# Optimization experiments

Hardware: AMD Instinct MI355X
Metric: run time of the kernel (lower is better)

The kernel has to match this reference:

```python
import jax, jax.numpy as jnp
import numpy as np

DIM = 256
HEADS = 8
W0, W1 = 8, 8
N = W0 * W1
SCALE = (DIM // HEADS) ** (-0.5)


def _rel_pos_index(w0, w1):
    ch = np.arange(w0)
    cw = np.arange(w1)
    coords = np.stack(np.meshgrid(ch, cw, indexing='ij')).reshape(2, -1)  # (2, N)
    rel = coords[:, :, None] - coords[:, None, :]                          # (2, N, N)
    rel = rel.transpose(1, 2, 0).copy()                                    # (N, N, 2)
    rel[:, :, 0] += w0 - 1
    rel[:, :, 1] += w1 - 1
    rel[:, :, 0] *= 2 * w1 - 1
    return rel.sum(-1)                                                     # (N, N)

REL_IDX = jnp.asarray(_rel_pos_index(W0, W1))


def setup_inputs() -> dict:
    key = jax.random.key(0)
    ks = jax.random.split(key, 9)
    B, C, H, W = 8, DIM, 128, 128
    s = DIM ** -0.5
    return {
        'x': jax.random.normal(ks[0], (B, C, H, W), jnp.float32),
        'embedding': jax.random.normal(ks[1], (1, N, DIM), jnp.float32),
        'rpb_table': jax.random.normal(ks[2], ((2 * W0 - 1) * (2 * W1 - 1), HEADS), jnp.float32),
        'q_w': jax.random.normal(ks[3], (DIM, DIM), jnp.float32) * s,
        'q_b': jnp.zeros((DIM,), jnp.float32),
        'kv_w': jax.random.normal(ks[4], (2 * DIM, DIM), jnp.float32) * s,
        'kv_b': jnp.zeros((2 * DIM,), jnp.float32),
        'proj_w': jax.random.normal(ks[5], (DIM, DIM), jnp.float32) * s,
        'proj_b': jnp.zeros((DIM,), jnp.float32),
    }


def reference(x, embedding, rpb_table, q_w, q_b, kv_w, kv_b, proj_w, proj_b):
    B, C, H, W = x.shape
    # window_partition (faithful to the original, incl. its discarded-permute view):
    # torch views the contiguous (B,C,H,W) buffer as (B, H//w0, w0, W//w1, w1, C)
    win = x.reshape(B, H // W0, W0, W // W1, W1, C)
    win = win.transpose(0, 1, 3, 2, 4, 5).reshape(-1, N, C)  # (Bw, N, C)
    Bw = win.shape[0]
    hd = C // HEADS

    q = jnp.einsum('bnc,dc->bnd', jnp.broadcast_to(embedding, (Bw, N, C)), q_w) + q_b
    q = q.reshape(Bw, N, HEADS, hd).transpose(0, 2, 1, 3)      # (Bw, h, N, hd)
    kv = jnp.einsum('bnc,dc->bnd', win, kv_w) + kv_b           # (Bw, N, 2C)
    kv = kv.reshape(Bw, N, 2, HEADS, hd).transpose(2, 0, 3, 1, 4)
    k, v = kv[0], kv[1]                                         # (Bw, h, N, hd)

    bias = rpb_table[REL_IDX.reshape(-1)].reshape(N, N, HEADS).transpose(2, 0, 1)  # (h, N, N)

    attn = jnp.einsum('bhnd,bhmd->bhnm', q * SCALE, k) + bias[None]
    attn = jax.nn.softmax(attn, axis=-1)
    out = jnp.einsum('bhnm,bhmd->bhnd', attn, v)
    out = out.transpose(0, 2, 1, 3).reshape(Bw, N, C)
    out = jnp.einsum('bnc,dc->bnd', out, proj_w) + proj_b
    return out
```

## Files before the change

### kernel.cpp

```cpp
#include <hip/hip_runtime.h>

typedef short bf16x8 __attribute__((ext_vector_type(8)));
typedef float f32x4 __attribute__((ext_vector_type(4)));
typedef float f32x16 __attribute__((ext_vector_type(16)));
typedef unsigned u32;
typedef unsigned short u16;
typedef unsigned u32x4v __attribute__((ext_vector_type(4)));
typedef unsigned u32x2v __attribute__((ext_vector_type(2)));

union UV { u32x4v u; bf16x8 v; };

__device__ __forceinline__ u16 f2bf(float f){
  u32 u = __float_as_uint(f);
  u += 0x7FFFu + ((u>>16)&1u);
  return (u16)(u>>16);
}
__device__ __forceinline__ u32 pack2(float lo, float hi){
  u32 r;
  asm("v_cvt_pk_bf16_f32 %0, %1, %2" : "=v"(r) : "v"(lo), "v"(hi));
  return r;
}

#define LOG2E 1.4426950408889634f

__global__ void k_prep(const float* __restrict__ emb, const float* __restrict__ q_w,
                       const float* __restrict__ q_b, u16* __restrict__ q_s,
                       const float* __restrict__ rpb, float* __restrict__ bias,
                       const float* __restrict__ kv_w, const float* __restrict__ proj_w,
                       u32* __restrict__ kvb, u32* __restrict__ pjb){
  const int blk = blockIdx.x, tid = threadIdx.x;
  if(blk < 64){
    const int n = blk, d = tid;
    const float4* er = (const float4*)(emb + n*256);
    const float4* wr = (const float4*)(q_w + d*256);
    float acc = 0.f;
    for(int c=0;c<64;++c){
      float4 e = er[c], w = wr[c];
      acc += e.x*w.x + e.y*w.y + e.z*w.z + e.w*w.w;
    }
    acc += q_b[d];
    q_s[n*256 + d] = f2bf(acc * (0.17677669529663687f * LOG2E));
  } else if(blk < 192){
    const int o = (blk-64)*256 + tid;
    const int h = o>>12, n = (o>>6)&63, m = o&63;
    const int idx = ((n>>3)-(m>>3)+7)*15 + ((n&7)-(m&7)+7);
    bias[o] = rpb[idx*8 + h] * LOG2E;
  } else {
    const int i = (blk-192)*256 + tid;
    if(i < 65536) kvb[i] = pack2(kv_w[2*i], kv_w[2*i+1]);
    else { int j = i - 65536; pjb[j] = pack2(proj_w[2*j], proj_w[2*j+1]); }
  }
}

__global__ __launch_bounds__(512,4) void k_fused(const float* __restrict__ x, const u16* __restrict__ kvw,
                                                 const float* __restrict__ kv_b, const u16* __restrict__ q_s,
                                                 const float* __restrict__ bias, const u16* __restrict__ pjw,
                                                 const float* __restrict__ proj_b, float* __restrict__ out){
  __shared__ char smem[65536];
  char* RA = smem;
  char* RB = smem + 32768;

  const int bw = blockIdx.x;
  const int b = bw>>8, h1 = (bw>>4)&15, w1 = bw&15;
  const int base = b*4194304 + h1*262144 + w1*2048;
  const int tid = threadIdx.x;
  const int w = tid>>6, l = tid&63, g = l>>4, li = l&15;
  const int l31 = l&31, hi = l>>5;

  const u16* wbase = kvw + (w*64 + li)*256 + g*8;
  bf16x8 bcur[4];
  #pragma unroll
  for(int ct=0;ct<4;++ct) bcur[ct] = *(const bf16x8*)(wbase + ct*4096);

  #pragma unroll
  for(int i=0;i<4;++i){
    int p = i*512 + tid;
    int n = p>>5;
    int c4 = (2*p)&63;
    const f32x4* gp = (const f32x4*)(x + base + (n>>3)*32768 + (n&7)*256 + c4*4);
    f32x4 lo = __builtin_nontemporal_load(gp);
    f32x4 hh = __builtin_nontemporal_load(gp+1);
    u32x4v d = { pack2(lo[0],lo[1]), pack2(lo[2],lo[3]), pack2(hh[0],hh[1]), pack2(hh[2],hh[3]) };
    *(u32x4v*)(RA + ((p*16) ^ ((n&7)<<4))) = d;
  }
  __syncthreads();

  f32x4 acc[4][4];
  #pragma unroll
  for(int ct=0;ct<4;++ct){
    float bv = kv_b[w*64 + ct*16 + li];
    #pragma unroll
    for(int rt=0;rt<4;++rt) acc[rt][ct] = (f32x4){bv,bv,bv,bv};
  }
  {
    __builtin_amdgcn_s_setprio(1);
    #pragma unroll
    for(int ks=0;ks<8;++ks){
      bf16x8 a[4];
      #pragma unroll
      for(int rt=0;rt<4;++rt){
        int n = rt*16 + li;
        a[rt] = *(const bf16x8*)(RA + ((n*512 + ks*64 + g*16) ^ ((n&7)<<4)));
      }
      #pragma unroll
      for(int ct=0;ct<4;++ct){
        #pragma unroll
        for(int rt=0;rt<4;++rt)
          acc[rt][ct] = __builtin_amdgcn_mfma_f32_16x16x32_bf16(a[rt], bcur[ct], acc[rt][ct], 0,0,0);
        if(ks<7) bcur[ct] = *(const bf16x8*)(wbase + ct*4096 + (ks+1)*32);
      }
    }
    __builtin_amdgcn_s_setprio(0);
  }
  __syncthreads();

  const int h = w;
  bf16x8 qf[2][2];
  #pragma unroll
  for(int nt=0;nt<2;++nt)
    #pragma unroll
    for(int ks=0;ks<2;++ks)
      qf[nt][ks] = *(const bf16x8*)(q_s + (nt*32 + l31)*256 + h*32 + ks*16 + hi*8);

  const int oddl = li & 1;
  if(w < 4){
    #pragma unroll
    for(int ct=0;ct<4;++ct){
      int colp = w*64 + ct*16 + (li & ~1);
      #pragma unroll
      for(int rt=0;rt<4;++rt){
        float v0=acc[rt][ct][0], v1=acc[rt][ct][1], v2=acc[rt][ct][2], v3=acc[rt][ct][3];
        float o0=__shfl_xor(v0,1), o1=__shfl_xor(v1,1), o2=__shfl_xor(v2,1), o3=__shfl_xor(v3,1);
        u32 d0 = oddl ? pack2(o2,v2) : pack2(v0,o0);
        u32 d1 = oddl ? pack2(o3,v3) : pack2(v1,o1);
        int row0 = rt*16 + 4*g + (oddl ? 2 : 0);
        *(u32*)(RA + ((row0*512     + colp*2) ^ ((row0&7)<<4)))     = d0;
        *(u32*)(RA + (((row0+1)*512 + colp*2) ^ (((row0+1)&7)<<4))) = d1;
      }
    }
  } else {
    #pragma unroll
    for(int ct=0;ct<4;++ct){
      int c2 = (w-4)*64 + ct*16 + li;
      int hv = c2>>5, e = c2&31;
      #pragma unroll
      for(int rt=0;rt<4;++rt){
        u32x2v d;
        d[0] = pack2(acc[rt][ct][0], acc[rt][ct][1]);
        d[1] = pack2(acc[rt][ct][2], acc[rt][ct][3]);
        int m0 = rt*16 + 4*g;
        *(u32x2v*)(RB + (((hv*32 + e)*128 + m0*2) ^ ((e&7)<<4))) = d;
      }
    }
  }
  __syncthreads();

  bf16x8 kf[2][2];
  #pragma unroll
  for(int mt=0;mt<2;++mt)
    #pragma unroll
    for(int ks=0;ks<2;++ks){
      int row = mt*32 + l31;
      kf[mt][ks] = *(const bf16x8*)(RA + ((row*512 + (h*32 + ks*16 + hi*8)*2) ^ ((row&7)<<4)));
    }

  f32x16 S[2][2];
  #pragma unroll
  for(int mt=0;mt<2;++mt)
    #pragma unroll
    for(int nt=0;nt<2;++nt){
      int n = nt*32 + l31;
      const float* bp = bias + h*4096 + n*64 + mt*32 + 4*hi;
      #pragma unroll
      for(int q=0;q<4;++q){
        float4 bv = *(const float4*)(bp + q*8);
        S[mt][nt][4*q+0] = bv.x; S[mt][nt][4*q+1] = bv.y;
        S[mt][nt][4*q+2] = bv.z; S[mt][nt][4*q+3] = bv.w;
      }
    }
  __builtin_amdgcn_s_setprio(1);
  #pragma unroll
  for(int ks=0;ks<2;++ks)
    #pragma unroll
    for(int mt=0;mt<2;++mt)
      #pragma unroll
      for(int nt=0;nt<2;++nt)
        S[mt][nt] = __builtin_amdgcn_mfma_f32_32x32x16_bf16(kf[mt][ks], qf[nt][ks], S[mt][nt], 0,0,0);
  __builtin_amdgcn_s_setprio(0);

  float rs[2];
  u32 cb0[2][8], cb1[2][8];
  #pragma unroll
  for(int nt=0;nt<2;++nt){
    float t[16];
    #pragma unroll
    for(int j=0;j<16;++j) t[j] = fmaxf(S[0][nt][j], S[1][nt][j]);
    float m0 = fmaxf(fmaxf(t[0],t[1]),t[2]);
    float m1 = fmaxf(fmaxf(t[3],t[4]),t[5]);
    float m2 = fmaxf(fmaxf(t[6],t[7]),t[8]);
    float m3 = fmaxf(fmaxf(t[9],t[10]),t[11]);
    float m4 = fmaxf(fmaxf(t[12],t[13]),t[14]);
    float mA = fmaxf(fmaxf(m0,m1),m2);
    float mB = fmaxf(fmaxf(m3,m4),t[15]);
    float ml = fmaxf(mA,mB);
    float mx = fmaxf(ml, __shfl_xor(ml, 32));
    float sm[16];
    #pragma unroll
    for(int j=0;j<16;++j){
      S[0][nt][j] = __builtin_amdgcn_exp2f(S[0][nt][j] - mx);
      S[1][nt][j] = __builtin_amdgcn_exp2f(S[1][nt][j] - mx);
      sm[j] = S[0][nt][j] + S[1][nt][j];
    }
    #pragma unroll
    for(int s=8;s>0;s>>=1)
      #pragma unroll
      for(int j=0;j<8;++j) if(j<s) sm[j] += sm[j+s];
    float total = sm[0] + __shfl_xor(sm[0], 32);
    rs[nt] = 1.0f/total;
    #pragma unroll
    for(int mt=0;mt<2;++mt)
      #pragma unroll
      for(int q=0;q<4;++q){
        cb0[nt][mt*4+q] = pack2(S[mt][nt][4*q+0], S[mt][nt][4*q+1]);
        cb1[nt][mt*4+q] = pack2(S[mt][nt][4*q+2], S[mt][nt][4*q+3]);
      }
  }

  f32x16 O[2];
  O[0] = (f32x16)(0.f); O[1] = (f32x16)(0.f);
  __builtin_amdgcn_s_setprio(1);
  #pragma unroll
  for(int ks2=0;ks2<4;++ks2){
    bf16x8 vf = *(const bf16x8*)(RB + (((h*32 + l31)*128 + (ks2*16 + hi*8)*2) ^ ((l31&7)<<4)));
    #pragma unroll
    for(int nt=0;nt<2;++nt){
      u32 A0 = cb0[nt][2*ks2], B0 = cb0[nt][2*ks2+1];
      u32 A1 = cb1[nt][2*ks2], B1 = cb1[nt][2*ks2+1];
      u32 r0 = (u32)__shfl_xor((int)(hi ? A0 : B0), 32);
      u32 r1 = (u32)__shfl_xor((int)(hi ? A1 : B1), 32);
      u32 w0 = hi ? r0 : A0;
      u32 w1 = hi ? r1 : A1;
      u32 w2 = hi ? B0 : r0;
      u32 w3 = hi ? B1 : r1;
      UV t; t.u = (u32x4v){w0,w1,w2,w3};
      O[nt] = __builtin_amdgcn_mfma_f32_32x32x16_bf16(vf, t.v, O[nt], 0,0,0);
    }
  }
  __builtin_amdgcn_s_setprio(0);

  const u16* pbase = pjw + (w*32 + li)*256 + g*8;
  bf16x8 bc[2];
  #pragma unroll
  for(int ct=0;ct<2;++ct) bc[ct] = *(const bf16x8*)(pbase + ct*4096);

  #pragma unroll
  for(int nt=0;nt<2;++nt){
    int n = nt*32 + l31;
    #pragma unroll
    for(int q=0;q<4;++q){
      u32x2v d;
      d[0] = pack2(O[nt][4*q+0]*rs[nt], O[nt][4*q+1]*rs[nt]);
      d[1] = pack2(O[nt][4*q+2]*rs[nt], O[nt][4*q+3]*rs[nt]);
      *(u32x2v*)(RB + h*4096 + ((n*64 + (8*q + 4*hi)*2) ^ ((n&7)<<4))) = d;
    }
  }
  __syncthreads();

  {
    f32x4 pacc[4][2];
    #pragma unroll
    for(int ct=0;ct<2;++ct){
      float bv = proj_b[w*32 + ct*16 + li];
      #pragma unroll
      for(int rt=0;rt<4;++rt) pacc[rt][ct] = (f32x4){bv,bv,bv,bv};
    }
    __builtin_amdgcn_s_setprio(1);
    #pragma unroll
    for(int ks=0;ks<8;++ks){
      bf16x8 a[4];
      #pragma unroll
      for(int rt=0;rt<4;++rt){
        int row = rt*16 + li;
        a[rt] = *(const bf16x8*)(RB + ks*4096 + ((row*64 + g*16) ^ ((row&7)<<4)));
      }
      #pragma unroll
      for(int ct=0;ct<2;++ct){
        #pragma unroll
        for(int rt=0;rt<4;++rt)
          pacc[rt][ct] = __builtin_amdgcn_mfma_f32_16x16x32_bf16(a[rt], bc[ct], pacc[rt][ct], 0,0,0);
        if(ks<7) bc[ct] = *(const bf16x8*)(pbase + ct*4096 + (ks+1)*32);
      }
    }
    __builtin_amdgcn_s_setprio(0);
    #pragma unroll
    for(int rt=0;rt<4;++rt)
      #pragma unroll
      for(int ct=0;ct<2;++ct)
        #pragma unroll
        for(int r=0;r<4;++r)
          __builtin_nontemporal_store(pacc[rt][ct][r],
            &out[(bw*64 + rt*16 + 4*g + r)*256 + w*32 + ct*16 + li]);
  }
}

extern "C" void kernel_launch(void* const* d_in, const int* in_sizes, int n_in,
                              void* d_out, int out_size, void* d_ws, size_t ws_size,
                              hipStream_t stream){
  (void)in_sizes; (void)n_in; (void)out_size;
  const float* x      = (const float*)d_in[0];
  const float* emb    = (const float*)d_in[1];
  const float* rpb    = (const float*)d_in[2];
  const float* q_w    = (const float*)d_in[3];
  const float* q_b    = (const float*)d_in[4];
  const float* kv_w   = (const float*)d_in[5];
  const float* kv_b   = (const float*)d_in[6];
  const float* proj_w = (const float*)d_in[7];
  const float* proj_b = (const float*)d_in[8];
  float* out = (float*)d_out;

  char* ws = (char*)d_ws;
  if(ws_size < (size_t)557056) return;
  u16* q_s   = (u16*)(ws);
  float* bias= (float*)(ws + 32768);
  u32* kvb   = (u32*)(ws + 163840);
  u32* pjb   = (u32*)(ws + 425984);

  k_prep <<< 576, 256, 0, stream>>>(emb, q_w, q_b, q_s, rpb, bias, kv_w, proj_w, kvb, pjb);
  k_fused<<<2048, 512, 0, stream>>>(x, (const u16*)kvb, kv_b, q_s, bias,
                                    (const u16*)pjb, proj_b, out);
}
```

Baseline: 355.1 us.

## Split x window load into two halves and overlap second half with MFMA

```diff
diff --git a/kernel.cpp b/kernel.cpp
--- a/kernel.cpp
+++ b/kernel.cpp
@@ -73,15 +73,23 @@
   for(int ct=0;ct<4;++ct) bcur[ct] = *(const bf16x8*)(wbase + ct*4096);
 
   #pragma unroll
-  for(int i=0;i<4;++i){
-    int p = i*512 + tid;
-    int n = p>>5;
-    int c4 = (2*p)&63;
-    const f32x4* gp = (const f32x4*)(x + base + (n>>3)*32768 + (n&7)*256 + c4*4);
+  for(int i=0;i<2;++i){
+    int q = i*512 + tid;
+    int n = q>>4, j = q&15;
+    const f32x4* gp = (const f32x4*)(x + base + (n>>3)*32768 + (n&7)*256 + j*8);
     f32x4 lo = __builtin_nontemporal_load(gp);
     f32x4 hh = __builtin_nontemporal_load(gp+1);
     u32x4v d = { pack2(lo[0],lo[1]), pack2(lo[2],lo[3]), pack2(hh[0],hh[1]), pack2(hh[2],hh[3]) };
-    *(u32x4v*)(RA + ((p*16) ^ ((n&7)<<4))) = d;
+    *(u32x4v*)(RA + ((n*512 + j*16) ^ ((n&7)<<4))) = d;
+  }
+  f32x4 xr[4];
+  #pragma unroll
+  for(int i=0;i<2;++i){
+    int q = i*512 + tid;
+    int n = q>>4, j = q&15;
+    const f32x4* gp = (const f32x4*)(x + base + (n>>3)*32768 + (n&7)*256 + 128 + j*8);
+    xr[i*2+0] = __builtin_nontemporal_load(gp);
+    xr[i*2+1] = __builtin_nontemporal_load(gp+1);
   }
   __syncthreads();
 
@@ -92,26 +100,51 @@
     #pragma unroll
     for(int rt=0;rt<4;++rt) acc[rt][ct] = (f32x4){bv,bv,bv,bv};
   }
-  {
-    __builtin_amdgcn_s_setprio(1);
-    #pragma unroll
-    for(int ks=0;ks<8;++ks){
-      bf16x8 a[4];
-      #pragma unroll
-      for(int rt=0;rt<4;++rt){
-        int n = rt*16 + li;
-        a[rt] = *(const bf16x8*)(RA + ((n*512 + ks*64 + g*16) ^ ((n&7)<<4)));
-      }
-      #pragma unroll
-      for(int ct=0;ct<4;++ct){
-        #pragma unroll
-        for(int rt=0;rt<4;++rt)
-          acc[rt][ct] = __builtin_amdgcn_mfma_f32_16x16x32_bf16(a[rt], bcur[ct], acc[rt][ct], 0,0,0);
-        if(ks<7) bcur[ct] = *(const bf16x8*)(wbase + ct*4096 + (ks+1)*32);
-      }
-    }
-    __builtin_amdgcn_s_setprio(0);
-  }
+  __builtin_amdgcn_s_setprio(1);
+  #pragma unroll
+  for(int ks=0;ks<4;++ks){
+    bf16x8 a[4];
+    #pragma unroll
+    for(int rt=0;rt<4;++rt){
+      int n = rt*16 + li;
+      a[rt] = *(const bf16x8*)(RA + ((n*512 + ks*64 + g*16) ^ ((n&7)<<4)));
+    }
+    #pragma unroll
+    for(int ct=0;ct<4;++ct){
+      #pragma unroll
+      for(int rt=0;rt<4;++rt)
+        acc[rt][ct] = __builtin_amdgcn_mfma_f32_16x16x32_bf16(a[rt], bcur[ct], acc[rt][ct], 0,0,0);
+      bcur[ct] = *(const bf16x8*)(wbase + ct*4096 + (ks+1)*32);
+    }
+  }
+  __builtin_amdgcn_s_setprio(0);
+  #pragma unroll
+  for(int i=0;i<2;++i){
+    int q = i*512 + tid;
+    int n = q>>4, j = q&15;
+    u32x4v d = { pack2(xr[i*2+0][0],xr[i*2+0][1]), pack2(xr[i*2+0][2],xr[i*2+0][3]),
+                 pack2(xr[i*2+1][0],xr[i*2+1][1]), pack2(xr[i*2+1][2],xr[i*2+1][3]) };
+    *(u32x4v*)(RA + ((n*512 + 256 + j*16) ^ ((n&7)<<4))) = d;
+  }
+  __syncthreads();
+  __builtin_amdgcn_s_setprio(1);
+  #pragma unroll
+  for(int ks=4;ks<8;++ks){
+    bf16x8 a[4];
+    #pragma unroll
+    for(int rt=0;rt<4;++rt){
+      int n = rt*16 + li;
+      a[rt] = *(const bf16x8*)(RA + ((n*512 + ks*64 + g*16) ^ ((n&7)<<4)));
+    }
+    #pragma unroll
+    for(int ct=0;ct<4;++ct){
+      #pragma unroll
+      for(int rt=0;rt<4;++rt)
+        acc[rt][ct] = __builtin_amdgcn_mfma_f32_16x16x32_bf16(a[rt], bcur[ct], acc[rt][ct], 0,0,0);
+      if(ks<7) bcur[ct] = *(const bf16x8*)(wbase + ct*4096 + (ks+1)*32);
+    }
+  }
+  __builtin_amdgcn_s_setprio(0);
   __syncthreads();
 
   const int h = w;
```

After: 358.9 us. Within noise of the previous version (+1.1%).
